# Performance work log

Hardware: AMD Instinct MI355X
Metric: run time of the kernel (lower is better)

## Reference

```python
import jax, jax.numpy as jnp
import numpy as np

N = 60000      # total atoms
E = 120000     # total directed bond edges
B = 1024       # molecules per batch
DIN = 88       # unpacked node feature bits
DE = 32        # unpacked edge feature bits
EMB = 256      # graph_dims
L = 4          # num MPNN layers
HID = 512      # attention hid_dim
H = 8          # n_heads
HD = HID // H  # head dim


def _bn(x, g, b):
    # BatchNorm1d in training mode: biased batch stats over dim 0
    m = x.mean(0)
    v = x.var(0)
    return g * (x - m) * jax.lax.rsqrt(v + 1e-5) + b


def setup_inputs() -> dict:
    ks = jax.random.split(jax.random.key(0), 24)
    p = lambda i, s: jax.random.normal(ks[i], s, jnp.float32) * 0.02
    z = lambda s: jnp.zeros(s, jnp.float32)
    o = lambda s: jnp.ones(s, jnp.float32)
    return {
        "x": jax.random.uniform(ks[0], (N, DIN), jnp.float32),
        "edge_index": jax.random.randint(ks[1], (2, E), 0, N),
        "edge_attr": jax.random.uniform(ks[2], (E, DE), jnp.float32),
        "batch": jnp.sort(jax.random.randint(ks[3], (N,), 0, B)),
        "fp": jax.random.uniform(ks[4], (B, 2048), jnp.float32),
        "target": (jax.random.uniform(ks[5], (B, 3)) > 0.5).astype(jnp.float32),
        "lin_w": p(6, (DIN, EMB)), "lin_b": z(EMB),
        "msg_w1": p(7, (L, 2 * EMB + DE, EMB)), "msg_b1": z((L, EMB)), "msg_g1": o((L, EMB)), "msg_be1": z((L, EMB)),
        "msg_w2": p(8, (L, EMB, EMB)), "msg_b2": z((L, EMB)), "msg_g2": o((L, EMB)), "msg_be2": z((L, EMB)),
        "upd_w1": p(9, (L, 2 * EMB, EMB)), "upd_b1": z((L, EMB)), "upd_g1": o((L, EMB)), "upd_be1": z((L, EMB)),
        "upd_w2": p(10, (L, EMB, EMB)), "upd_b2": z((L, EMB)), "upd_g2": o((L, EMB)), "upd_be2": z((L, EMB)),
        "gl_w1": p(11, (EMB, 1024)), "gl_b1": z(1024),
        "gl_w2": p(12, (1024, 1024)), "gl_b2": z(1024),
        "gl_w3": p(13, (1024, HID)), "gl_b3": z(HID),
        "fp_w": p(14, (2048, HID)), "fp_b": z(HID),
        "att_w": p(15, (2, 4, HID, HID)), "att_b": z((2, 4, HID)),
        "bind_w": p(16, (HID, 3)), "bind_b": z(3),
    }


def reference(x, edge_index, edge_attr, batch, fp, target,
              lin_w, lin_b,
              msg_w1, msg_b1, msg_g1, msg_be1, msg_w2, msg_b2, msg_g2, msg_be2,
              upd_w1, upd_b1, upd_g1, upd_be1, upd_w2, upd_b2, upd_g2, upd_be2,
              gl_w1, gl_b1, gl_w2, gl_b2, gl_w3, gl_b3,
              fp_w, fp_b, att_w, att_b, bind_w, bind_b):
    relu = jax.nn.relu
    src, dst = edge_index[0], edge_index[1]  # PyG: row 0 = source j, row 1 = target i
    h = x @ lin_w + lin_b  # (n, EMB)
    for l in range(msg_w1.shape[0]):
        # message: gather dst/src node feats + edge feats -> 2-layer BN MLP
        m = jnp.concatenate([h[dst], h[src], edge_attr], axis=-1)  # (e, 2*EMB+DE)
        m = relu(_bn(m @ msg_w1[l] + msg_b1[l], msg_g1[l], msg_be1[l]))
        m = relu(_bn(m @ msg_w2[l] + msg_b2[l], msg_g2[l], msg_be2[l]))
        # aggregate: scatter-add into destination nodes
        aggr = jax.ops.segment_sum(m, dst, num_segments=h.shape[0])  # (n, EMB)
        # update: concat with h -> 2-layer BN MLP; residual from MPNNModel
        u = jnp.concatenate([h, aggr], axis=-1)
        u = relu(_bn(u @ upd_w1[l] + upd_b1[l], upd_g1[l], upd_be1[l]))
        u = relu(_bn(u @ upd_w2[l] + upd_b2[l], upd_g2[l], upd_be2[l]))
        h = h + u
    # global mean pool per graph
    nb = fp.shape[0]
    sums = jax.ops.segment_sum(h, batch, num_segments=nb)
    cnt = jax.ops.segment_sum(jnp.ones((h.shape[0],), h.dtype), batch, num_segments=nb)
    g = sums / jnp.maximum(cnt, 1.0)[:, None]  # (B, EMB)
    # graph MLP (dropout = identity at inference)
    g = relu(g @ gl_w1 + gl_b1)
    g = relu(g @ gl_w2 + gl_b2)
    g = g @ gl_w3 + gl_b3  # (B, 512)
    fpf = relu(fp @ fp_w + fp_b)  # (B, 512)

    def attn(i, q, k, v):
        Q = (q @ att_w[i, 0] + att_b[i, 0]).reshape(-1, H, HD)
        K = (k @ att_w[i, 1] + att_b[i, 1]).reshape(-1, H, HD)
        V = (v @ att_w[i, 2] + att_b[i, 2]).reshape(-1, H, HD)
        # energy[b,h,d,e] = Q[b,h,d]*K[b,h,e] / sqrt(HD): outer product per head
        energy = jnp.einsum('bhd,bhe->bhde', Q, K) / jnp.sqrt(jnp.float32(HD))
        a = jax.nn.softmax(energy, axis=-1)
        o = jnp.einsum('bhde,bhe->bhd', a, V)
        # torch permute(0,2,1,3).view: flatten in (head_dim, head) order
        o = o.transpose(0, 2, 1).reshape(-1, H * HD)
        return o @ att_w[i, 3] + att_b[i, 3]

    g = g + attn(0, fpf, g, g)   # cross attention fp -> graph
    g = attn(1, g, g, g)          # self attention
    bind = g @ bind_w + bind_b    # (B, 3)
    # stable BCE-with-logits, mean reduction
    loss = jnp.mean(jnp.maximum(bind, 0.0) - bind * target + jnp.log1p(jnp.exp(-jnp.abs(bind))))
    return loss, jax.nn.sigmoid(bind)
```

## Files before the change

kernel.cpp:

```cpp
#include <hip/hip_runtime.h>
#include <hip/hip_bf16.h>
#include <math.h>

typedef long long i64;
typedef __hip_bfloat16 bf16;
typedef __attribute__((ext_vector_type(8))) short bfx8;
typedef __attribute__((ext_vector_type(4))) float f32x4;

#define NATOMS 60000
#define NEDGES 120000
#define NB     1024
#define EMB    256
#define NL     4
#define HIDF   512
#define NH     8
#define HD     64
#define SCANB  235

__device__ __forceinline__ void storeT(float* p, float v) { *p = v; }
__device__ __forceinline__ void storeT(bf16* p, float v) { *p = __float2bfloat16(v); }

__device__ __forceinline__ void gl_lds16(const void* g, void* l) {
  __builtin_amdgcn_global_load_lds((const __attribute__((address_space(1))) void*)g,
                                   (__attribute__((address_space(3))) void*)l, 16, 0, 0);
}

template<int MODE, typename TO>
__global__ __launch_bounds__(256, 2) void mgemm_k(
    const bf16* __restrict__ A, const bf16* __restrict__ A2,
    const int* __restrict__ gdst, const int* __restrict__ gsrc,
    const bf16* __restrict__ Wt,
    const float* __restrict__ bias, const float* __restrict__ resid,
    TO* __restrict__ C, float* __restrict__ stats,
    int M, int Kp, int N, int doRelu)
{
  __shared__ short As[128 * 64];
  __shared__ short Bs[128 * 64];
  __shared__ float sSum[128], sSq[128];

  const int tid = threadIdx.x;
  const int w = tid >> 6, lane = tid & 63;
  const int wr = w >> 1, wc = w & 1;
  const int row0 = blockIdx.y * 128, col0 = blockIdx.x * 128;

  int rI[4], slotG[4], dIdx[4], sIdx[4], rClamp[4];
  #pragma unroll
  for (int i = 0; i < 4; ++i) {
    int lin = i * 256 + tid;
    int r = lin >> 3, sl = lin & 7;
    rI[i] = r;
    slotG[i] = sl ^ (r & 7);
    rClamp[i] = min(row0 + r, M - 1);
    if (MODE == 1) { dIdx[i] = gdst[rClamp[i]]; sIdx[i] = gsrc[rClamp[i]]; }
  }

  f32x4 acc[4][4];
  #pragma unroll
  for (int a = 0; a < 4; ++a)
    #pragma unroll
    for (int b = 0; b < 4; ++b)
      acc[a][b] = (f32x4){0.f, 0.f, 0.f, 0.f};

  const int KT = Kp >> 6;
  for (int kt = 0; kt < KT; ++kt) {
    const int k0 = kt << 6;
    #pragma unroll
    for (int i = 0; i < 4; ++i) {
      const bf16* g;
      int ko = slotG[i] * 8;
      if constexpr (MODE == 0) {
        g = A + (i64)rClamp[i] * Kp + k0 + ko;
      } else if constexpr (MODE == 1) {
        if (k0 < 256)      g = A  + (i64)dIdx[i] * EMB + k0 + ko;
        else if (k0 < 512) g = A  + (i64)sIdx[i] * EMB + (k0 - 256) + ko;
        else               g = A2 + (i64)rClamp[i] * 64 + (k0 - 512) + ko;
      } else {
        g = (k0 < 256) ? A  + (i64)rClamp[i] * EMB + k0 + ko
                       : A2 + (i64)rClamp[i] * EMB + (k0 - 256) + ko;
      }
      gl_lds16(g, (char*)&As[0] + i * 4096 + w * 1024);
    }
    #pragma unroll
    for (int i = 0; i < 4; ++i) {
      const bf16* g = Wt + (i64)(col0 + rI[i]) * Kp + k0 + slotG[i] * 8;
      gl_lds16(g, (char*)&Bs[0] + i * 4096 + w * 1024);
    }
    __syncthreads();

    #pragma unroll
    for (int ks = 0; ks < 2; ++ks) {
      bfx8 af[4], bf_[4];
      #pragma unroll
      for (int mi = 0; mi < 4; ++mi) {
        int r = wr * 64 + mi * 16 + (lane & 15);
        int q = ks * 4 + (lane >> 4);
        int s = q ^ (r & 7);
        af[mi] = *(const bfx8*)&As[r * 64 + s * 8];
      }
      #pragma unroll
      for (int ni = 0; ni < 4; ++ni) {
        int n = wc * 64 + ni * 16 + (lane & 15);
        int q = ks * 4 + (lane >> 4);
        int s = q ^ (n & 7);
        bf_[ni] = *(const bfx8*)&Bs[n * 64 + s * 8];
      }
      #pragma unroll
      for (int mi = 0; mi < 4; ++mi)
        #pragma unroll
        for (int ni = 0; ni < 4; ++ni)
          acc[mi][ni] = __builtin_amdgcn_mfma_f32_16x16x32_bf16(af[mi], bf_[ni], acc[mi][ni], 0, 0, 0);
    }
    __syncthreads();
  }

  #pragma unroll
  for (int mi = 0; mi < 4; ++mi) {
    #pragma unroll
    for (int j = 0; j < 4; ++j) {
      int row = row0 + wr * 64 + mi * 16 + (lane >> 4) * 4 + j;
      if (row < M) {
        #pragma unroll
        for (int ni = 0; ni < 4; ++ni) {
          int col = col0 + wc * 64 + ni * 16 + (lane & 15);
          float v = acc[mi][ni][j];
          if (bias)  v += bias[col];
          if (resid) v += resid[(i64)row * N + col];
          if (doRelu) v = fmaxf(v, 0.f);
          storeT(&C[(i64)row * N + col], v);
        }
      }
    }
  }

  if (stats) {
    if (tid < 128) { sSum[tid] = 0.f; sSq[tid] = 0.f; }
    __syncthreads();
    #pragma unroll
    for (int ni = 0; ni < 4; ++ni) {
      float ps = 0.f, pq = 0.f;
      #pragma unroll
      for (int mi = 0; mi < 4; ++mi)
        #pragma unroll
        for (int j = 0; j < 4; ++j) {
          int row = row0 + wr * 64 + mi * 16 + (lane >> 4) * 4 + j;
          if (row < M) { float v = acc[mi][ni][j]; ps += v; pq += v * v; }
        }
      ps += __shfl_xor(ps, 16); ps += __shfl_xor(ps, 32);
      pq += __shfl_xor(pq, 16); pq += __shfl_xor(pq, 32);
      if (lane < 16) {
        int c = wc * 64 + ni * 16 + lane;
        atomicAdd(&sSum[c], ps); atomicAdd(&sSq[c], pq);
      }
    }
    __syncthreads();
    if (tid < 128) {
      atomicAdd(&stats[col0 + tid], sSum[tid]);
      atomicAdd(&stats[256 + col0 + tid], sSq[tid]);
    }
  }
}

struct WDesc { const float* W; bf16* Wt; int K, N, Kp, bStart; };
struct WPack { WDesc d[29]; int cnt; };

__global__ __launch_bounds__(256) void wcvt_k(WPack p) {
  int bid = blockIdx.x;
  int di = 0;
  for (int i = 1; i < 29; ++i) if (i < p.cnt && bid >= p.d[i].bStart) di = i;
  WDesc wd = p.d[di];
  int t = bid - wd.bStart;
  int tilesN = wd.N >> 5;
  int tn = t % tilesN, tk = t / tilesN;
  __shared__ float tl[32][33];
  int tx = threadIdx.x & 31, ty = threadIdx.x >> 5;
  #pragma unroll
  for (int ii = 0; ii < 4; ++ii) {
    int k = tk * 32 + ty + ii * 8;
    int n = tn * 32 + tx;
    tl[ty + ii * 8][tx] = (k < wd.K) ? wd.W[(i64)k * wd.N + n] : 0.f;
  }
  __syncthreads();
  #pragma unroll
  for (int ii = 0; ii < 4; ++ii) {
    int n = tn * 32 + ty + ii * 8;
    int k = tk * 32 + tx;
    wd.Wt[(i64)n * wd.Kp + k] = __float2bfloat16(tl[tx][ty + ii * 8]);
  }
}

__global__ void padcvt_k(const float* __restrict__ S, bf16* __restrict__ D,
                         int rows, int sc, int dc) {
  i64 total = (i64)rows * dc;
  for (i64 i = (i64)blockIdx.x * blockDim.x + threadIdx.x; i < total;
       i += (i64)gridDim.x * blockDim.x) {
    int r = (int)(i / dc), c = (int)(i % dc);
    D[i] = __float2bfloat16(c < sc ? S[(i64)r * sc + c] : 0.f);
  }
}

__global__ void cvt_k(const float* __restrict__ S, bf16* __restrict__ D, i64 total) {
  i64 i0 = ((i64)blockIdx.x * blockDim.x + threadIdx.x) * 4;
  i64 stride = (i64)gridDim.x * blockDim.x * 4;
  for (i64 i = i0; i < total; i += stride) {
    float4 v = *(const float4*)(S + i);
    D[i + 0] = __float2bfloat16(v.x);
    D[i + 1] = __float2bfloat16(v.y);
    D[i + 2] = __float2bfloat16(v.z);
    D[i + 3] = __float2bfloat16(v.w);
  }
}

template<int HASADD>
__global__ __launch_bounds__(256) void bnap_k(
    const bf16* __restrict__ X, const bf16* __restrict__ addIn, bf16* __restrict__ Y,
    const float* __restrict__ st, const float* __restrict__ gam, const float* __restrict__ bet,
    i64 total, float invM)
{
  __shared__ float sc[256], sh[256];
  {
    int c = threadIdx.x;
    float mean = st[c] * invM;
    float var  = st[256 + c] * invM - mean * mean;
    float rs   = rsqrtf(var + 1e-5f);
    float s    = gam[c] * rs;
    sc[c] = s; sh[c] = bet[c] - mean * s;
  }
  __syncthreads();
  i64 i0 = ((i64)blockIdx.x * blockDim.x + threadIdx.x) * 8;
  i64 stride = (i64)gridDim.x * blockDim.x * 8;
  for (i64 i = i0; i < total; i += stride) {
    bfx8 xv = *(const bfx8*)((const short*)X + i);
    bfx8 av;
    if (HASADD) av = *(const bfx8*)((const short*)addIn + i);
    int c0 = (int)(i & 255);
    bfx8 o;
    #pragma unroll
    for (int j = 0; j < 8; ++j) {
      unsigned short u = (unsigned short)xv[j];
      float x = __bfloat162float(*reinterpret_cast<const bf16*>(&u));
      int c = c0 + j;
      float t = fmaxf(x * sc[c] + sh[c], 0.f);
      if (HASADD) {
        unsigned short ua = (unsigned short)av[j];
        t += __bfloat162float(*reinterpret_cast<const bf16*>(&ua));
      }
      bf16 b = __float2bfloat16(t);
      o[j] = (short)*reinterpret_cast<unsigned short*>(&b);
    }
    *(bfx8*)((short*)Y + i) = o;
  }
}

__global__ void deg_k(const int* __restrict__ dst, int* __restrict__ deg) {
  int e = blockIdx.x * blockDim.x + threadIdx.x;
  if (e < NEDGES) atomicAdd(&deg[dst[e]], 1);
}

__global__ __launch_bounds__(256) void scanA_k(const int* __restrict__ deg, int* __restrict__ bsum) {
  __shared__ int sh[256];
  int i = blockIdx.x * 256 + threadIdx.x;
  sh[threadIdx.x] = (i < NATOMS) ? deg[i] : 0;
  __syncthreads();
  for (int s = 128; s > 0; s >>= 1) {
    if (threadIdx.x < s) sh[threadIdx.x] += sh[threadIdx.x + s];
    __syncthreads();
  }
  if (threadIdx.x == 0) bsum[blockIdx.x] = sh[0];
}

__global__ __launch_bounds__(256) void scanB_k(int* __restrict__ bsum) {
  __shared__ int sh[256];
  int v = (threadIdx.x < SCANB) ? bsum[threadIdx.x] : 0;
  sh[threadIdx.x] = v;
  __syncthreads();
  for (int ofs = 1; ofs < 256; ofs <<= 1) {
    int t = (threadIdx.x >= ofs) ? sh[threadIdx.x - ofs] : 0;
    __syncthreads();
    sh[threadIdx.x] += t;
    __syncthreads();
  }
  if (threadIdx.x < SCANB) bsum[threadIdx.x] = sh[threadIdx.x] - v;
}

__global__ __launch_bounds__(256) void scanC_k(const int* __restrict__ deg,
                                               const int* __restrict__ bsum,
                                               int* __restrict__ starts,
                                               int* __restrict__ cursor) {
  __shared__ int sh[256];
  int i = blockIdx.x * 256 + threadIdx.x;
  int v = (i < NATOMS) ? deg[i] : 0;
  sh[threadIdx.x] = v;
  __syncthreads();
  for (int ofs = 1; ofs < 256; ofs <<= 1) {
    int t = (threadIdx.x >= ofs) ? sh[threadIdx.x - ofs] : 0;
    __syncthreads();
    sh[threadIdx.x] += t;
    __syncthreads();
  }
  int excl = bsum[blockIdx.x] + sh[threadIdx.x] - v;
  if (i < NATOMS) { starts[i] = excl; cursor[i] = excl; }
  if (i == NATOMS - 1) starts[NATOMS] = NEDGES;
}

__global__ void fill_k(const int* __restrict__ dst, int* __restrict__ cursor,
                       int* __restrict__ elist) {
  int e = blockIdx.x * blockDim.x + threadIdx.x;
  if (e < NEDGES) { int pos = atomicAdd(&cursor[dst[e]], 1); elist[pos] = e; }
}

__global__ __launch_bounds__(256) void gather_k(
    const bf16* __restrict__ m2, const int* __restrict__ starts,
    const int* __restrict__ elist,
    const float* __restrict__ st, const float* __restrict__ gam,
    const float* __restrict__ bet, float invM, bf16* __restrict__ aggrb)
{
  const int c = threadIdx.x;
  float mean = st[c] * invM;
  float var  = st[256 + c] * invM - mean * mean;
  float rs   = rsqrtf(var + 1e-5f);
  float scv  = gam[c] * rs;
  float shv  = bet[c] - mean * scv;
  for (int n = blockIdx.x; n < NATOMS; n += gridDim.x) {
    int s = starts[n], e = starts[n + 1];
    float acc = 0.f;
    for (int i = s; i < e; ++i) {
      int eid = elist[i];
      float v = __bfloat162float(m2[(i64)eid * EMB + c]);
      acc += fmaxf(v * scv + shv, 0.f);
    }
    aggrb[(i64)n * EMB + c] = __float2bfloat16(acc);
  }
}

__global__ __launch_bounds__(256) void pool_seg_k(const bf16* __restrict__ h,
                                                  const int* __restrict__ batch,
                                                  bf16* __restrict__ g0b) {
  int b = blockIdx.x, c = threadIdx.x;
  int lo = 0, hi = NATOMS;
  while (lo < hi) { int mid = (lo + hi) >> 1; if (batch[mid] < b) lo = mid + 1; else hi = mid; }
  int s = lo;
  hi = NATOMS;
  while (lo < hi) { int mid = (lo + hi) >> 1; if (batch[mid] < b + 1) lo = mid + 1; else hi = mid; }
  int e = lo;
  float acc = 0.f;
  for (int r = s; r < e; ++r) acc += __bfloat162float(h[(i64)r * EMB + c]);
  g0b[b * EMB + c] = __float2bfloat16(acc / (float)max(e - s, 1));
}

__global__ __launch_bounds__(64) void attn_k(const float* __restrict__ Q, const float* __restrict__ K,
                                             const float* __restrict__ V, bf16* __restrict__ O) {
  int b = blockIdx.x >> 3, hh = blockIdx.x & 7;
  int d = threadIdx.x;
  __shared__ float Ks[HD], Vs[HD];
  Ks[d] = K[(i64)b * HIDF + hh * HD + d];
  Vs[d] = V[(i64)b * HIDF + hh * HD + d];
  __syncthreads();
  float q = Q[(i64)b * HIDF + hh * HD + d] * 0.125f;
  float mx = -1e30f;
  #pragma unroll
  for (int e = 0; e < HD; ++e) mx = fmaxf(mx, q * Ks[e]);
  float s = 0.f, o = 0.f;
  #pragma unroll
  for (int e = 0; e < HD; ++e) {
    float p = expf(q * Ks[e] - mx);
    s += p; o += p * Vs[e];
  }
  O[(i64)b * HIDF + d * NH + hh] = __float2bfloat16(o / s);
}

__global__ __launch_bounds__(256) void bind_loss_k(const float* __restrict__ g, const float* __restrict__ W,
                                                   const float* __restrict__ bb, const float* __restrict__ tgt,
                                                   float* __restrict__ out) {
  int gt = blockIdx.x * 256 + threadIdx.x;
  int r = gt >> 3, sub = gt & 7;
  float a0 = 0.f, a1 = 0.f, a2 = 0.f;
  const float* gr = g + (i64)r * HIDF + sub * 64;
  for (int k = 0; k < 64; ++k) {
    float gv = gr[k];
    const float* wr_ = W + (sub * 64 + k) * 3;
    a0 += gv * wr_[0];
    a1 += gv * wr_[1];
    a2 += gv * wr_[2];
  }
  #pragma unroll
  for (int ofs = 4; ofs > 0; ofs >>= 1) {
    a0 += __shfl_down(a0, ofs, 8);
    a1 += __shfl_down(a1, ofs, 8);
    a2 += __shfl_down(a2, ofs, 8);
  }
  float lsum = 0.f;
  if (sub == 0) {
    float bv[3] = {a0 + bb[0], a1 + bb[1], a2 + bb[2]};
    #pragma unroll
    for (int j = 0; j < 3; ++j) {
      float xv = bv[j], t = tgt[r * 3 + j];
      lsum += fmaxf(xv, 0.f) - xv * t + log1pf(expf(-fabsf(xv)));
      out[1 + r * 3 + j] = 1.f / (1.f + expf(-xv));
    }
  }
  __shared__ float red[256];
  red[threadIdx.x] = lsum;
  __syncthreads();
  for (int s = 128; s > 0; s >>= 1) {
    if (threadIdx.x < s) red[threadIdx.x] += red[threadIdx.x + s];
    __syncthreads();
  }
  if (threadIdx.x == 0) atomicAdd(&out[0], red[0] * (1.f / (NB * 3)));
}

extern "C" void kernel_launch(void* const* d_in, const int* in_sizes, int n_in,
                              void* d_out, int out_size, void* d_ws, size_t ws_size,
                              hipStream_t stream) {
  const float* x         = (const float*)d_in[0];
  const int*   ei        = (const int*)  d_in[1];
  const float* edge_attr = (const float*)d_in[2];
  const int*   batch     = (const int*)  d_in[3];
  const float* fp        = (const float*)d_in[4];
  const float* target    = (const float*)d_in[5];
  const float* lin_w     = (const float*)d_in[6];
  const float* lin_b     = (const float*)d_in[7];
  const float* msg_w1    = (const float*)d_in[8];
  const float* msg_g1    = (const float*)d_in[10];
  const float* msg_be1   = (const float*)d_in[11];
  const float* msg_w2    = (const float*)d_in[12];
  const float* msg_g2    = (const float*)d_in[14];
  const float* msg_be2   = (const float*)d_in[15];
  const float* upd_w1    = (const float*)d_in[16];
  const float* upd_g1    = (const float*)d_in[18];
  const float* upd_be1   = (const float*)d_in[19];
  const float* upd_w2    = (const float*)d_in[20];
  const float* upd_g2    = (const float*)d_in[22];
  const float* upd_be2   = (const float*)d_in[23];
  const float* gl_w1     = (const float*)d_in[24];
  const float* gl_b1     = (const float*)d_in[25];
  const float* gl_w2     = (const float*)d_in[26];
  const float* gl_b2     = (const float*)d_in[27];
  const float* gl_w3     = (const float*)d_in[28];
  const float* gl_b3     = (const float*)d_in[29];
  const float* fp_w      = (const float*)d_in[30];
  const float* fp_b      = (const float*)d_in[31];
  const float* att_w     = (const float*)d_in[32];
  const float* att_b     = (const float*)d_in[33];
  const float* bind_w    = (const float*)d_in[34];
  const float* bind_b    = (const float*)d_in[35];

  const int* src = ei;
  const int* dst = ei + NEDGES;

  char* base = (char*)d_ws;
  float* stats = (float*)base;
  char* p = base + 8192 * 4;
  int* deg    = (int*)p; p += 60000 * 4;
  int* starts = (int*)p; p += 60004 * 4;
  int* cursor = (int*)p; p += 60000 * 4;
  int* elist  = (int*)p; p += 120000 * 4;
  int* bsum   = (int*)p; p += 256 * 4;
  bf16* h_bf  = (bf16*)p; p += (i64)NATOMS * EMB * 2;
  bf16* ea_bf = (bf16*)p; p += (i64)NEDGES * 64 * 2;
  bf16* wt    = (bf16*)p; p += 6651904LL * 2;
  char* R1 = p; p += 61440000LL;
  char* R2 = p;

  bf16* Wt_lin = wt; wt += 256 * 128;
  bf16 *Wt_m1[NL], *Wt_m2[NL], *Wt_u1[NL], *Wt_u2[NL];
  for (int l = 0; l < NL; ++l) { Wt_m1[l] = wt; wt += 256 * 576; }
  for (int l = 0; l < NL; ++l) { Wt_m2[l] = wt; wt += 256 * 256; }
  for (int l = 0; l < NL; ++l) { Wt_u1[l] = wt; wt += 256 * 512; }
  for (int l = 0; l < NL; ++l) { Wt_u2[l] = wt; wt += 256 * 256; }
  bf16* Wt_gl1 = wt; wt += 1024 * 256;
  bf16* Wt_gl2 = wt; wt += 1024 * 1024;
  bf16* Wt_gl3 = wt; wt += 512 * 1024;
  bf16* Wt_fp  = wt; wt += 512 * 2048;
  bf16* Wt_att[8];
  for (int i = 0; i < 8; ++i) { Wt_att[i] = wt; wt += 512 * 512; }

  bf16*  x_bf  = (bf16*)R2;
  bf16*  m1b   = (bf16*)R1;
  bf16*  m2b   = (bf16*)R2;
  bf16*  aggrb = (bf16*)R1;
  bf16*  u1b   = (bf16*)R2;
  bf16*  u2b   = (bf16*)R1;

  bf16*  g0b  = (bf16*)R1;
  bf16*  gh1b = g0b + (i64)NB * EMB;
  bf16*  gh2b = gh1b + (i64)NB * 1024;
  float* g3   = (float*)(gh2b + (i64)NB * 1024);
  bf16*  g3b  = (bf16*)(g3 + (i64)NB * HIDF);
  bf16*  fpb  = g3b + (i64)NB * HIDF;
  bf16*  fpfb = fpb + (i64)NB * 2048;
  float* Qb   = (float*)(fpfb + (i64)NB * HIDF);
  float* Kb   = Qb + (i64)NB * HIDF;
  float* Vb   = Kb + (i64)NB * HIDF;
  bf16*  Obb  = (bf16*)(Vb + (i64)NB * HIDF);
  float* gc1  = (float*)(Obb + (i64)NB * HIDF);
  bf16*  gc1b = (bf16*)(gc1 + (i64)NB * HIDF);
  float* gc2  = (float*)(gc1b + (i64)NB * HIDF);

  hipMemsetAsync(stats, 0, (8192 + 60000) * 4, stream);
  hipMemsetAsync(d_out, 0, 4, stream);

  deg_k<<<(NEDGES + 255) / 256, 256, 0, stream>>>(dst, deg);
  scanA_k<<<SCANB, 256, 0, stream>>>(deg, bsum);
  scanB_k<<<1, 256, 0, stream>>>(bsum);
  scanC_k<<<SCANB, 256, 0, stream>>>(deg, bsum, starts, cursor);
  fill_k<<<(NEDGES + 255) / 256, 256, 0, stream>>>(dst, cursor, elist);

  WPack pk; int bs = 0, di = 0;
  auto addW = [&](const float* Wp, bf16* Wtp, int K, int N, int Kp) {
    pk.d[di].W = Wp; pk.d[di].Wt = Wtp; pk.d[di].K = K; pk.d[di].N = N;
    pk.d[di].Kp = Kp; pk.d[di].bStart = bs;
    bs += (Kp / 32) * (N / 32); ++di;
  };
  addW(lin_w, Wt_lin, 88, 256, 128);
  for (int l = 0; l < NL; ++l) addW(msg_w1 + (i64)l * 544 * 256, Wt_m1[l], 544, 256, 576);
  for (int l = 0; l < NL; ++l) addW(msg_w2 + (i64)l * 256 * 256, Wt_m2[l], 256, 256, 256);
  for (int l = 0; l < NL; ++l) addW(upd_w1 + (i64)l * 512 * 256, Wt_u1[l], 512, 256, 512);
  for (int l = 0; l < NL; ++l) addW(upd_w2 + (i64)l * 256 * 256, Wt_u2[l], 256, 256, 256);
  addW(gl_w1, Wt_gl1, 256, 1024, 256);
  addW(gl_w2, Wt_gl2, 1024, 1024, 1024);
  addW(gl_w3, Wt_gl3, 1024, 512, 1024);
  addW(fp_w, Wt_fp, 2048, 512, 2048);
  for (int i = 0; i < 8; ++i) addW(att_w + (i64)i * 512 * 512, Wt_att[i], 512, 512, 512);
  pk.cnt = di;
  wcvt_k<<<bs, 256, 0, stream>>>(pk);

  padcvt_k<<<2048, 256, 0, stream>>>(x, x_bf, NATOMS, 88, 128);
  padcvt_k<<<2048, 256, 0, stream>>>(edge_attr, ea_bf, NEDGES, 32, 64);

  dim3 gE(2, (NEDGES + 127) / 128), gN(2, (NATOMS + 127) / 128);

  mgemm_k<0, bf16><<<gN, 256, 0, stream>>>(x_bf, nullptr, nullptr, nullptr, Wt_lin,
      lin_b, nullptr, h_bf, nullptr, NATOMS, 128, 256, 0);

  for (int l = 0; l < NL; ++l) {
    float* st0 = stats + (l * 4 + 0) * 512;
    float* st1 = stats + (l * 4 + 1) * 512;
    float* st2 = stats + (l * 4 + 2) * 512;
    float* st3 = stats + (l * 4 + 3) * 512;
    mgemm_k<1, bf16><<<gE, 256, 0, stream>>>(h_bf, ea_bf, dst, src, Wt_m1[l],
        nullptr, nullptr, m1b, st0, NEDGES, 576, 256, 0);
    bnap_k<0><<<2048, 256, 0, stream>>>(m1b, nullptr, m1b, st0,
        msg_g1 + l * EMB, msg_be1 + l * EMB, (i64)NEDGES * EMB, 1.f / NEDGES);
    mgemm_k<0, bf16><<<gE, 256, 0, stream>>>(m1b, nullptr, nullptr, nullptr, Wt_m2[l],
        nullptr, nullptr, m2b, st1, NEDGES, 256, 256, 0);
    gather_k<<<2048, 256, 0, stream>>>(m2b, starts, elist, st1,
        msg_g2 + l * EMB, msg_be2 + l * EMB, 1.f / NEDGES, aggrb);
    mgemm_k<2, bf16><<<gN, 256, 0, stream>>>(h_bf, aggrb, nullptr, nullptr, Wt_u1[l],
        nullptr, nullptr, u1b, st2, NATOMS, 512, 256, 0);
    bnap_k<0><<<2048, 256, 0, stream>>>(u1b, nullptr, u1b, st2,
        upd_g1 + l * EMB, upd_be1 + l * EMB, (i64)NATOMS * EMB, 1.f / NATOMS);
    mgemm_k<0, bf16><<<gN, 256, 0, stream>>>(u1b, nullptr, nullptr, nullptr, Wt_u2[l],
        nullptr, nullptr, u2b, st3, NATOMS, 256, 256, 0);
    bnap_k<1><<<2048, 256, 0, stream>>>(u2b, h_bf, h_bf, st3,
        upd_g2 + l * EMB, upd_be2 + l * EMB, (i64)NATOMS * EMB, 1.f / NATOMS);
  }

  pool_seg_k<<<NB, 256, 0, stream>>>(h_bf, batch, g0b);

  mgemm_k<0, bf16><<<dim3(8, 8), 256, 0, stream>>>(g0b, nullptr, nullptr, nullptr, Wt_gl1,
      gl_b1, nullptr, gh1b, nullptr, NB, 256, 1024, 1);
  mgemm_k<0, bf16><<<dim3(8, 8), 256, 0, stream>>>(gh1b, nullptr, nullptr, nullptr, Wt_gl2,
      gl_b2, nullptr, gh2b, nullptr, NB, 1024, 1024, 1);
  mgemm_k<0, float><<<dim3(4, 8), 256, 0, stream>>>(gh2b, nullptr, nullptr, nullptr, Wt_gl3,
      gl_b3, nullptr, g3, nullptr, NB, 1024, 512, 0);
  cvt_k<<<512, 256, 0, stream>>>(g3, g3b, (i64)NB * HIDF);
  cvt_k<<<512, 256, 0, stream>>>(fp, fpb, (i64)NB * 2048);
  mgemm_k<0, bf16><<<dim3(4, 8), 256, 0, stream>>>(fpb, nullptr, nullptr, nullptr, Wt_fp,
      fp_b, nullptr, fpfb, nullptr, NB, 2048, 512, 1);

  mgemm_k<0, float><<<dim3(4, 8), 256, 0, stream>>>(fpfb, nullptr, nullptr, nullptr, Wt_att[0],
      att_b + 0 * HIDF, nullptr, Qb, nullptr, NB, 512, 512, 0);
  mgemm_k<0, float><<<dim3(4, 8), 256, 0, stream>>>(g3b, nullptr, nullptr, nullptr, Wt_att[1],
      att_b + 1 * HIDF, nullptr, Kb, nullptr, NB, 512, 512, 0);
  mgemm_k<0, float><<<dim3(4, 8), 256, 0, stream>>>(g3b, nullptr, nullptr, nullptr, Wt_att[2],
      att_b + 2 * HIDF, nullptr, Vb, nullptr, NB, 512, 512, 0);
  attn_k<<<NB * NH, 64, 0, stream>>>(Qb, Kb, Vb, Obb);
  mgemm_k<0, float><<<dim3(4, 8), 256, 0, stream>>>(Obb, nullptr, nullptr, nullptr, Wt_att[3],
      att_b + 3 * HIDF, g3, gc1, nullptr, NB, 512, 512, 0);
  cvt_k<<<512, 256, 0, stream>>>(gc1, gc1b, (i64)NB * HIDF);

  mgemm_k<0, float><<<dim3(4, 8), 256, 0, stream>>>(gc1b, nullptr, nullptr, nullptr, Wt_att[4],
      att_b + 4 * HIDF, nullptr, Qb, nullptr, NB, 512, 512, 0);
  mgemm_k<0, float><<<dim3(4, 8), 256, 0, stream>>>(gc1b, nullptr, nullptr, nullptr, Wt_att[5],
      att_b + 5 * HIDF, nullptr, Kb, nullptr, NB, 512, 512, 0);
  mgemm_k<0, float><<<dim3(4, 8), 256, 0, stream>>>(gc1b, nullptr, nullptr, nullptr, Wt_att[6],
      att_b + 6 * HIDF, nullptr, Vb, nullptr, NB, 512, 512, 0);
  attn_k<<<NB * NH, 64, 0, stream>>>(Qb, Kb, Vb, Obb);
  mgemm_k<0, float><<<dim3(4, 8), 256, 0, stream>>>(Obb, nullptr, nullptr, nullptr, Wt_att[7],
      att_b + 7 * HIDF, nullptr, gc2, nullptr, NB, 512, 512, 0);

  bind_loss_k<<<32, 256, 0, stream>>>(gc2, bind_w, bind_b, target, (float*)d_out);
}
```

Baseline: 1.861 ms.

## Widen GEMM tile to full 256 columns and fuse BN-ReLU into A-load

The GEMM tile grows from 128x128 to 128x256, so each block covers all 256 output columns and the gathered or concatenated A rows are read once instead of twice. The first BatchNorm+ReLU of the message and update MLPs is folded into the following GEMM's A-operand load, applied from stats in registers and written to LDS, which drops two standalone elementwise passes per layer. The cost is twice the accumulator registers and B-tile LDS, which may lower occupancy. The fused path also replaces async global-to-LDS copies with synchronous register loads.

```diff
diff --git a/kernel.cpp b/kernel.cpp
--- a/kernel.cpp
+++ b/kernel.cpp
@@ -19,77 +19,120 @@
 
 __device__ __forceinline__ void storeT(float* p, float v) { *p = v; }
 __device__ __forceinline__ void storeT(bf16* p, float v) { *p = __float2bfloat16(v); }
+__device__ __forceinline__ float b2f(short u) {
+  unsigned short us = (unsigned short)u;
+  return __bfloat162float(*reinterpret_cast<const bf16*>(&us));
+}
+__device__ __forceinline__ short f2b(float f) {
+  bf16 b = __float2bfloat16(f);
+  return (short)*reinterpret_cast<unsigned short*>(&b);
+}
 
 __device__ __forceinline__ void gl_lds16(const void* g, void* l) {
   __builtin_amdgcn_global_load_lds((const __attribute__((address_space(1))) void*)g,
                                    (__attribute__((address_space(3))) void*)l, 16, 0, 0);
 }
 
-template<int MODE, typename TO>
+template<int MODE, int AFFINE, typename TO>
 __global__ __launch_bounds__(256, 2) void mgemm_k(
     const bf16* __restrict__ A, const bf16* __restrict__ A2,
     const int* __restrict__ gdst, const int* __restrict__ gsrc,
     const bf16* __restrict__ Wt,
     const float* __restrict__ bias, const float* __restrict__ resid,
     TO* __restrict__ C, float* __restrict__ stats,
+    const float* __restrict__ aff_st, const float* __restrict__ aff_g,
+    const float* __restrict__ aff_b, float aff_invM,
     int M, int Kp, int N, int doRelu)
 {
   __shared__ short As[128 * 64];
-  __shared__ short Bs[128 * 64];
-  __shared__ float sSum[128], sSq[128];
+  __shared__ short Bs[256 * 64];
+  __shared__ float sSum[256], sSq[256];
+  __shared__ float aSc[256], aSh[256];
 
   const int tid = threadIdx.x;
   const int w = tid >> 6, lane = tid & 63;
   const int wr = w >> 1, wc = w & 1;
-  const int row0 = blockIdx.y * 128, col0 = blockIdx.x * 128;
-
-  int rI[4], slotG[4], dIdx[4], sIdx[4], rClamp[4];
+  const int row0 = blockIdx.y * 128, col0 = blockIdx.x * 256;
+
+  if constexpr (AFFINE) {
+    int c = tid;
+    float mean = aff_st[c] * aff_invM;
+    float var  = aff_st[256 + c] * aff_invM - mean * mean;
+    float rs   = rsqrtf(var + 1e-5f);
+    float s    = aff_g[c] * rs;
+    aSc[c] = s; aSh[c] = aff_b[c] - mean * s;
+    __syncthreads();
+  }
+
+  int slotG[4], dIdx[4], sIdx[4], rClamp[4];
   #pragma unroll
   for (int i = 0; i < 4; ++i) {
     int lin = i * 256 + tid;
     int r = lin >> 3, sl = lin & 7;
-    rI[i] = r;
     slotG[i] = sl ^ (r & 7);
     rClamp[i] = min(row0 + r, M - 1);
     if (MODE == 1) { dIdx[i] = gdst[rClamp[i]]; sIdx[i] = gsrc[rClamp[i]]; }
   }
-
-  f32x4 acc[4][4];
+  int rB[8], slB[8];
+  #pragma unroll
+  for (int i = 0; i < 8; ++i) {
+    int lin = i * 256 + tid;
+    int r = lin >> 3;
+    rB[i] = r;
+    slB[i] = (lin & 7) ^ (r & 7);
+  }
+
+  f32x4 acc[4][8];
   #pragma unroll
   for (int a = 0; a < 4; ++a)
     #pragma unroll
-    for (int b = 0; b < 4; ++b)
+    for (int b = 0; b < 8; ++b)
       acc[a][b] = (f32x4){0.f, 0.f, 0.f, 0.f};
 
   const int KT = Kp >> 6;
   for (int kt = 0; kt < KT; ++kt) {
     const int k0 = kt << 6;
+    if constexpr (AFFINE) {
+      #pragma unroll
+      for (int i = 0; i < 4; ++i) {
+        bfx8 raw = *(const bfx8*)(A + (i64)rClamp[i] * 256 + k0 + slotG[i] * 8);
+        int cb = k0 + slotG[i] * 8;
+        bfx8 o;
+        #pragma unroll
+        for (int j = 0; j < 8; ++j) {
+          float v = fmaxf(b2f(raw[j]) * aSc[cb + j] + aSh[cb + j], 0.f);
+          o[j] = f2b(v);
+        }
+        *(bfx8*)((char*)&As[0] + (i * 256 + tid) * 16) = o;
+      }
+    } else {
+      #pragma unroll
+      for (int i = 0; i < 4; ++i) {
+        const bf16* g;
+        int ko = slotG[i] * 8;
+        if constexpr (MODE == 0) {
+          g = A + (i64)rClamp[i] * Kp + k0 + ko;
+        } else if constexpr (MODE == 1) {
+          if (k0 < 256)      g = A  + (i64)dIdx[i] * EMB + k0 + ko;
+          else if (k0 < 512) g = A  + (i64)sIdx[i] * EMB + (k0 - 256) + ko;
+          else               g = A2 + (i64)rClamp[i] * 64 + (k0 - 512) + ko;
+        } else {
+          g = (k0 < 256) ? A  + (i64)rClamp[i] * EMB + k0 + ko
+                         : A2 + (i64)rClamp[i] * EMB + (k0 - 256) + ko;
+        }
+        gl_lds16(g, (char*)&As[0] + i * 4096 + w * 1024);
+      }
+    }
     #pragma unroll
-    for (int i = 0; i < 4; ++i) {
-      const bf16* g;
-      int ko = slotG[i] * 8;
-      if constexpr (MODE == 0) {
-        g = A + (i64)rClamp[i] * Kp + k0 + ko;
-      } else if constexpr (MODE == 1) {
-        if (k0 < 256)      g = A  + (i64)dIdx[i] * EMB + k0 + ko;
-        else if (k0 < 512) g = A  + (i64)sIdx[i] * EMB + (k0 - 256) + ko;
-        else               g = A2 + (i64)rClamp[i] * 64 + (k0 - 512) + ko;
-      } else {
-        g = (k0 < 256) ? A  + (i64)rClamp[i] * EMB + k0 + ko
-                       : A2 + (i64)rClamp[i] * EMB + (k0 - 256) + ko;
-      }
-      gl_lds16(g, (char*)&As[0] + i * 4096 + w * 1024);
-    }
-    #pragma unroll
-    for (int i = 0; i < 4; ++i) {
-      const bf16* g = Wt + (i64)(col0 + rI[i]) * Kp + k0 + slotG[i] * 8;
+    for (int i = 0; i < 8; ++i) {
+      const bf16* g = Wt + (i64)(col0 + rB[i]) * Kp + k0 + slB[i] * 8;
       gl_lds16(g, (char*)&Bs[0] + i * 4096 + w * 1024);
     }
     __syncthreads();
 
     #pragma unroll
     for (int ks = 0; ks < 2; ++ks) {
-      bfx8 af[4], bf_[4];
+      bfx8 af[4], bf_[8];
       #pragma unroll
       for (int mi = 0; mi < 4; ++mi) {
         int r = wr * 64 + mi * 16 + (lane & 15);
@@ -98,8 +141,8 @@
         af[mi] = *(const bfx8*)&As[r * 64 + s * 8];
       }
       #pragma unroll
-      for (int ni = 0; ni < 4; ++ni) {
-        int n = wc * 64 + ni * 16 + (lane & 15);
+      for (int ni = 0; ni < 8; ++ni) {
+        int n = wc * 128 + ni * 16 + (lane & 15);
         int q = ks * 4 + (lane >> 4);
         int s = q ^ (n & 7);
         bf_[ni] = *(const bfx8*)&Bs[n * 64 + s * 8];
@@ -107,7 +150,7 @@
       #pragma unroll
       for (int mi = 0; mi < 4; ++mi)
         #pragma unroll
-        for (int ni = 0; ni < 4; ++ni)
+        for (int ni = 0; ni < 8; ++ni)
           acc[mi][ni] = __builtin_amdgcn_mfma_f32_16x16x32_bf16(af[mi], bf_[ni], acc[mi][ni], 0, 0, 0);
     }
     __syncthreads();
@@ -120,8 +163,8 @@
       int row = row0 + wr * 64 + mi * 16 + (lane >> 4) * 4 + j;
       if (row < M) {
         #pragma unroll
-        for (int ni = 0; ni < 4; ++ni) {
-          int col = col0 + wc * 64 + ni * 16 + (lane & 15);
+        for (int ni = 0; ni < 8; ++ni) {
+          int col = col0 + wc * 128 + ni * 16 + (lane & 15);
           float v = acc[mi][ni][j];
           if (bias)  v += bias[col];
           if (resid) v += resid[(i64)row * N + col];
@@ -133,10 +176,10 @@
   }
 
   if (stats) {
-    if (tid < 128) { sSum[tid] = 0.f; sSq[tid] = 0.f; }
+    sSum[tid] = 0.f; sSq[tid] = 0.f;
     __syncthreads();
     #pragma unroll
-    for (int ni = 0; ni < 4; ++ni) {
+    for (int ni = 0; ni < 8; ++ni) {
       float ps = 0.f, pq = 0.f;
       #pragma unroll
       for (int mi = 0; mi < 4; ++mi)
@@ -148,15 +191,13 @@
       ps += __shfl_xor(ps, 16); ps += __shfl_xor(ps, 32);
       pq += __shfl_xor(pq, 16); pq += __shfl_xor(pq, 32);
       if (lane < 16) {
-        int c = wc * 64 + ni * 16 + lane;
+        int c = wc * 128 + ni * 16 + lane;
         atomicAdd(&sSum[c], ps); atomicAdd(&sSq[c], pq);
       }
     }
     __syncthreads();
-    if (tid < 128) {
-      atomicAdd(&stats[col0 + tid], sSum[tid]);
-      atomicAdd(&stats[256 + col0 + tid], sSq[tid]);
-    }
+    atomicAdd(&stats[tid], sSum[tid]);
+    atomicAdd(&stats[256 + tid], sSq[tid]);
   }
 }
 
@@ -210,8 +251,7 @@
   }
 }
 
-template<int HASADD>
-__global__ __launch_bounds__(256) void bnap_k(
+__global__ __launch_bounds__(256) void bnap_add_k(
     const bf16* __restrict__ X, const bf16* __restrict__ addIn, bf16* __restrict__ Y,
     const float* __restrict__ st, const float* __restrict__ gam, const float* __restrict__ bet,
     i64 total, float invM)
@@ -230,22 +270,14 @@
   i64 stride = (i64)gridDim.x * blockDim.x * 8;
   for (i64 i = i0; i < total; i += stride) {
     bfx8 xv = *(const bfx8*)((const short*)X + i);
-    bfx8 av;
-    if (HASADD) av = *(const bfx8*)((const short*)addIn + i);
+    bfx8 av = *(const bfx8*)((const short*)addIn + i);
     int c0 = (int)(i & 255);
     bfx8 o;
     #pragma unroll
     for (int j = 0; j < 8; ++j) {
-      unsigned short u = (unsigned short)xv[j];
-      float x = __bfloat162float(*reinterpret_cast<const bf16*>(&u));
       int c = c0 + j;
-      float t = fmaxf(x * sc[c] + sh[c], 0.f);
-      if (HASADD) {
-        unsigned short ua = (unsigned short)av[j];
-        t += __bfloat162float(*reinterpret_cast<const bf16*>(&ua));
-      }
-      bf16 b = __float2bfloat16(t);
-      o[j] = (short)*reinterpret_cast<unsigned short*>(&b);
+      float t = fmaxf(b2f(xv[j]) * sc[c] + sh[c], 0.f) + b2f(av[j]);
+      o[j] = f2b(t);
     }
     *(bfx8*)((short*)Y + i) = o;
   }
@@ -527,67 +559,66 @@
   padcvt_k<<<2048, 256, 0, stream>>>(x, x_bf, NATOMS, 88, 128);
   padcvt_k<<<2048, 256, 0, stream>>>(edge_attr, ea_bf, NEDGES, 32, 64);
 
-  dim3 gE(2, (NEDGES + 127) / 128), gN(2, (NATOMS + 127) / 128);
-
-  mgemm_k<0, bf16><<<gN, 256, 0, stream>>>(x_bf, nullptr, nullptr, nullptr, Wt_lin,
-      lin_b, nullptr, h_bf, nullptr, NATOMS, 128, 256, 0);
+  dim3 gE(1, (NEDGES + 127) / 128), gN(1, (NATOMS + 127) / 128);
+  const float* nf = nullptr;
+
+  mgemm_k<0, 0, bf16><<<gN, 256, 0, stream>>>(x_bf, nullptr, nullptr, nullptr, Wt_lin,
+      lin_b, nullptr, h_bf, nullptr, nf, nf, nf, 0.f, NATOMS, 128, 256, 0);
 
   for (int l = 0; l < NL; ++l) {
     float* st0 = stats + (l * 4 + 0) * 512;
     float* st1 = stats + (l * 4 + 1) * 512;
     float* st2 = stats + (l * 4 + 2) * 512;
     float* st3 = stats + (l * 4 + 3) * 512;
-    mgemm_k<1, bf16><<<gE, 256, 0, stream>>>(h_bf, ea_bf, dst, src, Wt_m1[l],
-        nullptr, nullptr, m1b, st0, NEDGES, 576, 256, 0);
-    bnap_k<0><<<2048, 256, 0, stream>>>(m1b, nullptr, m1b, st0,
-        msg_g1 + l * EMB, msg_be1 + l * EMB, (i64)NEDGES * EMB, 1.f / NEDGES);
-    mgemm_k<0, bf16><<<gE, 256, 0, stream>>>(m1b, nullptr, nullptr, nullptr, Wt_m2[l],
-        nullptr, nullptr, m2b, st1, NEDGES, 256, 256, 0);
+    mgemm_k<1, 0, bf16><<<gE, 256, 0, stream>>>(h_bf, ea_bf, dst, src, Wt_m1[l],
+        nullptr, nullptr, m1b, st0, nf, nf, nf, 0.f, NEDGES, 576, 256, 0);
+    mgemm_k<0, 1, bf16><<<gE, 256, 0, stream>>>(m1b, nullptr, nullptr, nullptr, Wt_m2[l],
+        nullptr, nullptr, m2b, st1, st0, msg_g1 + l * EMB, msg_be1 + l * EMB, 1.f / NEDGES,
+        NEDGES, 256, 256, 0);
     gather_k<<<2048, 256, 0, stream>>>(m2b, starts, elist, st1,
         msg_g2 + l * EMB, msg_be2 + l * EMB, 1.f / NEDGES, aggrb);
-    mgemm_k<2, bf16><<<gN, 256, 0, stream>>>(h_bf, aggrb, nullptr, nullptr, Wt_u1[l],
-        nullptr, nullptr, u1b, st2, NATOMS, 512, 256, 0);
-    bnap_k<0><<<2048, 256, 0, stream>>>(u1b, nullptr, u1b, st2,
-        upd_g1 + l * EMB, upd_be1 + l * EMB, (i64)NATOMS * EMB, 1.f / NATOMS);
-    mgemm_k<0, bf16><<<gN, 256, 0, stream>>>(u1b, nullptr, nullptr, nullptr, Wt_u2[l],
-        nullptr, nullptr, u2b, st3, NATOMS, 256, 256, 0);
-    bnap_k<1><<<2048, 256, 0, stream>>>(u2b, h_bf, h_bf, st3,
+    mgemm_k<2, 0, bf16><<<gN, 256, 0, stream>>>(h_bf, aggrb, nullptr, nullptr, Wt_u1[l],
+        nullptr, nullptr, u1b, st2, nf, nf, nf, 0.f, NATOMS, 512, 256, 0);
+    mgemm_k<0, 1, bf16><<<gN, 256, 0, stream>>>(u1b, nullptr, nullptr, nullptr, Wt_u2[l],
+        nullptr, nullptr, u2b, st3, st2, upd_g1 + l * EMB, upd_be1 + l * EMB, 1.f / NATOMS,
+        NATOMS, 256, 256, 0);
+    bnap_add_k<<<2048, 256, 0, stream>>>(u2b, h_bf, h_bf, st3,
         upd_g2 + l * EMB, upd_be2 + l * EMB, (i64)NATOMS * EMB, 1.f / NATOMS);
   }
 
   pool_seg_k<<<NB, 256, 0, stream>>>(h_bf, batch, g0b);
 
-  mgemm_k<0, bf16><<<dim3(8, 8), 256, 0, stream>>>(g0b, nullptr, nullptr, nullptr, Wt_gl1,
-      gl_b1, nullptr, gh1b, nullptr, NB, 256, 1024, 1);
-  mgemm_k<0, bf16><<<dim3(8, 8), 256, 0, stream>>>(gh1b, nullptr, nullptr, nullptr, Wt_gl2,
-      gl_b2, nullptr, gh2b, nullptr, NB, 1024, 1024, 1);
-  mgemm_k<0, float><<<dim3(4, 8), 256, 0, stream>>>(gh2b, nullptr, nullptr, nullptr, Wt_gl3,
-      gl_b3, nullptr, g3, nullptr, NB, 1024, 512, 0);
+  mgemm_k<0, 0, bf16><<<dim3(4, 8), 256, 0, stream>>>(g0b, nullptr, nullptr, nullptr, Wt_gl1,
+      gl_b1, nullptr, gh1b, nullptr, nf, nf, nf, 0.f, NB, 256, 1024, 1);
+  mgemm_k<0, 0, bf16><<<dim3(4, 8), 256, 0, stream>>>(gh1b, nullptr, nullptr, nullptr, Wt_gl2,
+      gl_b2, nullptr, gh2b, nullptr, nf, nf, nf, 0.f, NB, 1024, 1024, 1);
+  mgemm_k<0, 0, float><<<dim3(2, 8), 256, 0, stream>>>(gh2b, nullptr, nullptr, nullptr, Wt_gl3,
+      gl_b3, nullptr, g3, nullptr, nf, nf, nf, 0.f, NB, 1024, 512, 0);
   cvt_k<<<512, 256, 0, stream>>>(g3, g3b, (i64)NB * HIDF);
   cvt_k<<<512, 256, 0, stream>>>(fp, fpb, (i64)NB * 2048);
-  mgemm_k<0, bf16><<<dim3(4, 8), 256, 0, stream>>>(fpb, nullptr, nullptr, nullptr, Wt_fp,
-      fp_b, nullptr, fpfb, nullptr, NB, 2048, 512, 1);
-
-  mgemm_k<0, float><<<dim3(4, 8), 256, 0, stream>>>(fpfb, nullptr, nullptr, nullptr, Wt_att[0],
-      att_b + 0 * HIDF, nullptr, Qb, nullptr, NB, 512, 512, 0);
-  mgemm_k<0, float><<<dim3(4, 8), 256, 0, stream>>>(g3b, nullptr, nullptr, nullptr, Wt_att[1],
-      att_b + 1 * HIDF, nullptr, Kb, nullptr, NB, 512, 512, 0);
-  mgemm_k<0, float><<<dim3(4, 8), 256, 0, stream>>>(g3b, nullptr, nullptr, nullptr, Wt_att[2],
-      att_b + 2 * HIDF, nullptr, Vb, nullptr, NB, 512, 512, 0);
+  mgemm_k<0, 0, bf16><<<dim3(2, 8), 256, 0, stream>>>(fpb, nullptr, nullptr, nullptr, Wt_fp,
+      fp_b, nullptr, fpfb, nullptr, nf, nf, nf, 0.f, NB, 2048, 512, 1);
+
+  mgemm_k<0, 0, float><<<dim3(2, 8), 256, 0, stream>>>(fpfb, nullptr, nullptr, nullptr, Wt_att[0],
+      att_b + 0 * HIDF, nullptr, Qb, nullptr, nf, nf, nf, 0.f, NB, 512, 512, 0);
+  mgemm_k<0, 0, float><<<dim3(2, 8), 256, 0, stream>>>(g3b, nullptr, nullptr, nullptr, Wt_att[1],
+      att_b + 1 * HIDF, nullptr, Kb, nullptr, nf, nf, nf, 0.f, NB, 512, 512, 0);
+  mgemm_k<0, 0, float><<<dim3(2, 8), 256, 0, stream>>>(g3b, nullptr, nullptr, nullptr, Wt_att[2],
+      att_b + 2 * HIDF, nullptr, Vb, nullptr, nf, nf, nf, 0.f, NB, 512, 512, 0);
   attn_k<<<NB * NH, 64, 0, stream>>>(Qb, Kb, Vb, Obb);
-  mgemm_k<0, float><<<dim3(4, 8), 256, 0, stream>>>(Obb, nullptr, nullptr, nullptr, Wt_att[3],
-      att_b + 3 * HIDF, g3, gc1, nullptr, NB, 512, 512, 0);
+  mgemm_k<0, 0, float><<<dim3(2, 8), 256, 0, stream>>>(Obb, nullptr, nullptr, nullptr, Wt_att[3],
+      att_b + 3 * HIDF, g3, gc1, nullptr, nf, nf, nf, 0.f, NB, 512, 512, 0);
   cvt_k<<<512, 256, 0, stream>>>(gc1, gc1b, (i64)NB * HIDF);
 
-  mgemm_k<0, float><<<dim3(4, 8), 256, 0, stream>>>(gc1b, nullptr, nullptr, nullptr, Wt_att[4],
-      att_b + 4 * HIDF, nullptr, Qb, nullptr, NB, 512, 512, 0);
-  mgemm_k<0, float><<<dim3(4, 8), 256, 0, stream>>>(gc1b, nullptr, nullptr, nullptr, Wt_att[5],
-      att_b + 5 * HIDF, nullptr, Kb, nullptr, NB, 512, 512, 0);
-  mgemm_k<0, float><<<dim3(4, 8), 256, 0, stream>>>(gc1b, nullptr, nullptr, nullptr, Wt_att[6],
-      att_b + 6 * HIDF, nullptr, Vb, nullptr, NB, 512, 512, 0);
+  mgemm_k<0, 0, float><<<dim3(2, 8), 256, 0, stream>>>(gc1b, nullptr, nullptr, nullptr, Wt_att[4],
+      att_b + 4 * HIDF, nullptr, Qb, nullptr, nf, nf, nf, 0.f, NB, 512, 512, 0);
+  mgemm_k<0, 0, float><<<dim3(2, 8), 256, 0, stream>>>(gc1b, nullptr, nullptr, nullptr, Wt_att[5],
+      att_b + 5 * HIDF, nullptr, Kb, nullptr, nf, nf, nf, 0.f, NB, 512, 512, 0);
+  mgemm_k<0, 0, float><<<dim3(2, 8), 256, 0, stream>>>(gc1b, nullptr, nullptr, nullptr, Wt_att[6],
+      att_b + 6 * HIDF, nullptr, Vb, nullptr, nf, nf, nf, 0.f, NB, 512, 512, 0);
   attn_k<<<NB * NH, 64, 0, stream>>>(Qb, Kb, Vb, Obb);
-  mgemm_k<0, float><<<dim3(4, 8), 256, 0, stream>>>(Obb, nullptr, nullptr, nullptr, Wt_att[7],
-      att_b + 7 * HIDF, nullptr, gc2, nullptr, NB, 512, 512, 0);
+  mgemm_k<0, 0, float><<<dim3(2, 8), 256, 0, stream>>>(Obb, nullptr, nullptr, nullptr, Wt_att[7],
+      att_b + 7 * HIDF, nullptr, gc2, nullptr, nf, nf, nf, 0.f, NB, 512, 512, 0);
 
   bind_loss_k<<<32, 256, 0, stream>>>(gc2, bind_w, bind_b, target, (float*)d_out);
 }
```

New measurement: 1.971 ms. +5.9%, slower.
